# Performance work log

Hardware: AMD Instinct MI355X
Metric: run time of the kernel (lower is better)

The kernel has to match this reference:

```python
import jax, jax.numpy as jnp
import numpy as np
import math

NUM_HEADS = 16
ROPE_BASE = 10000.0


def apply_rope(t):
    # t: [B, H, S, D] with D even. Interleaved-pair rotary embedding (torchtune-style).
    D = t.shape[-1]
    S = t.shape[-2]
    inv_freq = 1.0 / (ROPE_BASE ** (jnp.arange(0, D, 2, dtype=jnp.float32) / D))  # [D/2]
    angles = jnp.arange(S, dtype=jnp.float32)[:, None] * inv_freq[None, :]  # [S, D/2]
    cos = jnp.cos(angles).astype(t.dtype)  # [S, D/2]
    sin = jnp.sin(angles).astype(t.dtype)
    t1 = t[..., 0::2]  # [B, H, S, D/2]
    t2 = t[..., 1::2]
    r1 = t1 * cos - t2 * sin
    r2 = t1 * sin + t2 * cos
    # interleave back
    out = jnp.stack([r1, r2], axis=-1).reshape(t.shape)
    return out


def setup_inputs() -> dict:
    key = jax.random.key(0)
    ks = jax.random.split(key, 6)
    B, S, D = 4, 2048, 2048
    s_in = 1.0 / math.sqrt(D)
    x = jax.random.normal(ks[0], (B, S, D), dtype=jnp.float32)
    wq = jax.random.normal(ks[1], (D, D), dtype=jnp.float32) * s_in
    wk = jax.random.normal(ks[2], (D, D), dtype=jnp.float32) * s_in
    wv = jax.random.normal(ks[3], (D, D), dtype=jnp.float32) * s_in
    wo = jax.random.normal(ks[4], (D, D), dtype=jnp.float32) * s_in
    bo = jnp.zeros((D,), dtype=jnp.float32)
    return {"x": x, "wq": wq, "wk": wk, "wv": wv, "wo": wo, "bo": bo}


def reference(x, wq, wk, wv, wo, bo):
    B, S, D = x.shape
    H = NUM_HEADS
    hd = D // H
    # QKV projections (nn.Linear: y = x @ W^T)
    q = (x @ wq.T).reshape(B, S, H, hd).transpose(0, 2, 1, 3)  # [B,H,S,hd]
    k = (x @ wk.T).reshape(B, S, H, hd).transpose(0, 2, 1, 3)
    v = (x @ wv.T).reshape(B, S, H, hd).transpose(0, 2, 1, 3)
    q = apply_rope(q)
    k = apply_rope(k)
    # causal SDPA (dropout_p = 0 in eval)
    scale = 1.0 / math.sqrt(hd)
    scores = jnp.einsum('bhqd,bhkd->bhqk', q, k) * scale  # [B,H,S,S]
    causal = jnp.tril(jnp.ones((S, S), dtype=bool))
    scores = jnp.where(causal, scores, jnp.finfo(scores.dtype).min)
    attn = jax.nn.softmax(scores, axis=-1)
    ctx = jnp.einsum('bhqk,bhkd->bqhd', attn, v).reshape(B, S, D)
    return ctx @ wo.T + bo
```

## Files before the change

kernel.cpp:

```cpp
#include <hip/hip_runtime.h>

typedef short short8 __attribute__((ext_vector_type(8)));
typedef float f32x4 __attribute__((ext_vector_type(4)));
typedef unsigned int u32x4 __attribute__((ext_vector_type(4)));
typedef unsigned short u16x4 __attribute__((ext_vector_type(4)));
typedef unsigned short u16x8 __attribute__((ext_vector_type(8)));

__device__ __forceinline__ unsigned short f2bf(float f) {
  unsigned int u = __builtin_bit_cast(unsigned int, f);
  u += 0x7fffu + ((u >> 16) & 1u);
  return (unsigned short)(u >> 16);
}
__device__ __forceinline__ float bf2f(unsigned short h) {
  unsigned int u = ((unsigned int)h) << 16;
  return __builtin_bit_cast(float, u);
}

__device__ __forceinline__ void gl16(const unsigned short* g, unsigned short* l) {
  __builtin_amdgcn_global_load_lds((const __attribute__((address_space(1))) unsigned int*)g,
                                   (__attribute__((address_space(3))) unsigned int*)l, 16, 0, 0);
}

#define BB 4
#define SS 2048
#define DD 2048
#define HH 16
#define HD 128
#define MM (BB * SS)

__global__ void cast_all(const float* __restrict__ x, const float* __restrict__ wq,
                         const float* __restrict__ wk, const float* __restrict__ wv,
                         const float* __restrict__ wo, unsigned short* __restrict__ xb,
                         unsigned short* __restrict__ wqb, unsigned short* __restrict__ wkb,
                         unsigned short* __restrict__ wvb, unsigned short* __restrict__ wob) {
  int i = blockIdx.x * blockDim.x + threadIdx.x;
  const int X4 = (MM * DD) / 4;
  const int W4 = (DD * DD) / 4;
  const float* src;
  unsigned short* dst;
  int off;
  if (i < X4) {
    src = x; dst = xb; off = i;
  } else {
    int t = i - X4;
    int w = t >> 20;
    off = t & (W4 - 1);
    src = (w == 0) ? wq : (w == 1) ? wk : (w == 2) ? wv : wo;
    dst = (w == 0) ? wqb : (w == 1) ? wkb : (w == 2) ? wvb : wob;
  }
  f32x4 v = ((const f32x4*)src)[off];
  u16x4 o;
  o[0] = f2bf(v[0]); o[1] = f2bf(v[1]); o[2] = f2bf(v[2]); o[3] = f2bf(v[3]);
  ((u16x4*)dst)[off] = o;
}

#define STGH(P, R0, t, h, moff)                                                     \
  do {                                                                              \
    const unsigned short* _s =                                                      \
        (P) + (size_t)((R0) + (h) * 128 + srow) * DD + (size_t)((t) * 64 + scol);   \
    gl16(_s, lds + (moff) + (h) * 8192 + wvi * 512);                                \
    gl16(_s + (size_t)64 * DD, lds + (moff) + (h) * 8192 + 4096 + wvi * 512);       \
  } while (0)

#define BARRIER asm volatile("s_barrier" ::: "memory")

__device__ __forceinline__ void gemm_core(const unsigned short* __restrict__ Ap,
                                          const unsigned short* __restrict__ Bp,
                                          unsigned short* lds, int rt, int ct,
                                          f32x4 (&acc)[8][4]) {
  const int tid = threadIdx.x;
  const int lane = tid & 63, wvi = tid >> 6;
  const int wm = wvi >> 2, wn = wvi & 3;
  const int quad = lane >> 4, l16 = lane & 15;
  const int srow = wvi * 8 + (lane >> 3);
  const int scol = ((lane & 7) ^ (lane >> 3)) << 3;
  const int ck0 = (quad ^ (l16 & 7)) << 3;
  const int ck1 = ((4 + quad) ^ (l16 & 7)) << 3;
  const int aro = (wm * 128 + l16) << 6;
  const int bro = (wn * 64 + l16) << 6;
  const int rb = rt * 256, cb = ct * 256;

#pragma unroll
  for (int i = 0; i < 8; ++i)
#pragma unroll
    for (int j = 0; j < 4; ++j) acc[i][j] = f32x4{0.f, 0.f, 0.f, 0.f};

  STGH(Bp, cb, 0, 0, 16384);
  STGH(Bp, cb, 0, 1, 16384);
  STGH(Ap, rb, 0, 0, 0);
  STGH(Ap, rb, 0, 1, 0);
  STGH(Bp, cb, 1, 0, 49152);
  STGH(Bp, cb, 1, 1, 49152);
  asm volatile("s_waitcnt vmcnt(4)" ::: "memory");
  BARRIER;

#pragma unroll 2
  for (int t = 0; t < 32; ++t) {
    const unsigned short* ab = lds + ((t & 1) << 15);
    const unsigned short* bb = ab + 16384;
    const int pn = ((t + 1) & 1) << 15;
    const int pc = ((t & 1) << 15) + 16384;
    short8 aq[4][2], b0f[2][2], b1f[2][2];

#pragma unroll
    for (int mi = 0; mi < 4; ++mi) {
      aq[mi][0] = __builtin_bit_cast(short8, *(const u32x4*)(ab + aro + mi * 1024 + ck0));
      aq[mi][1] = __builtin_bit_cast(short8, *(const u32x4*)(ab + aro + mi * 1024 + ck1));
    }
#pragma unroll
    for (int ni = 0; ni < 2; ++ni) {
      b0f[ni][0] = __builtin_bit_cast(short8, *(const u32x4*)(bb + bro + ni * 1024 + ck0));
      b0f[ni][1] = __builtin_bit_cast(short8, *(const u32x4*)(bb + bro + ni * 1024 + ck1));
    }
    if (t < 31) STGH(Ap, rb, t + 1, 0, pn);
    BARRIER;
    __builtin_amdgcn_s_setprio(1);
#pragma unroll
    for (int k = 0; k < 2; ++k)
#pragma unroll
      for (int mi = 0; mi < 4; ++mi)
#pragma unroll
        for (int ni = 0; ni < 2; ++ni)
          acc[mi][ni] =
              __builtin_amdgcn_mfma_f32_16x16x32_bf16(aq[mi][k], b0f[ni][k], acc[mi][ni], 0, 0, 0);
    __builtin_amdgcn_s_setprio(0);
    BARRIER;

#pragma unroll
    for (int ni = 0; ni < 2; ++ni) {
      b1f[ni][0] = __builtin_bit_cast(short8, *(const u32x4*)(bb + bro + 2048 + ni * 1024 + ck0));
      b1f[ni][1] = __builtin_bit_cast(short8, *(const u32x4*)(bb + bro + 2048 + ni * 1024 + ck1));
    }
    if (t < 31) STGH(Ap, rb, t + 1, 1, pn);
    BARRIER;
    __builtin_amdgcn_s_setprio(1);
#pragma unroll
    for (int k = 0; k < 2; ++k)
#pragma unroll
      for (int mi = 0; mi < 4; ++mi)
#pragma unroll
        for (int ni = 0; ni < 2; ++ni)
          acc[mi][2 + ni] = __builtin_amdgcn_mfma_f32_16x16x32_bf16(aq[mi][k], b1f[ni][k],
                                                                    acc[mi][2 + ni], 0, 0, 0);
    __builtin_amdgcn_s_setprio(0);
    BARRIER;

#pragma unroll
    for (int mi = 0; mi < 4; ++mi) {
      aq[mi][0] = __builtin_bit_cast(short8, *(const u32x4*)(ab + aro + 4096 + mi * 1024 + ck0));
      aq[mi][1] = __builtin_bit_cast(short8, *(const u32x4*)(ab + aro + 4096 + mi * 1024 + ck1));
    }
    if (t < 30) STGH(Bp, cb, t + 2, 0, pc);
    BARRIER;
    __builtin_amdgcn_s_setprio(1);
#pragma unroll
    for (int k = 0; k < 2; ++k)
#pragma unroll
      for (int mi = 0; mi < 4; ++mi)
#pragma unroll
        for (int ni = 0; ni < 2; ++ni)
          acc[4 + mi][2 + ni] = __builtin_amdgcn_mfma_f32_16x16x32_bf16(
              aq[mi][k], b1f[ni][k], acc[4 + mi][2 + ni], 0, 0, 0);
    __builtin_amdgcn_s_setprio(0);
    BARRIER;

    if (t < 30) STGH(Bp, cb, t + 2, 1, pc);
    BARRIER;
    __builtin_amdgcn_s_setprio(1);
#pragma unroll
    for (int k = 0; k < 2; ++k)
#pragma unroll
      for (int mi = 0; mi < 4; ++mi)
#pragma unroll
        for (int ni = 0; ni < 2; ++ni)
          acc[4 + mi][ni] = __builtin_amdgcn_mfma_f32_16x16x32_bf16(aq[mi][k], b0f[ni][k],
                                                                    acc[4 + mi][ni], 0, 0, 0);
    __builtin_amdgcn_s_setprio(0);
    if (t < 30) {
      asm volatile("s_waitcnt vmcnt(4)" ::: "memory");
      BARRIER;
    } else if (t == 30) {
      asm volatile("s_waitcnt vmcnt(0)" ::: "memory");
      BARRIER;
    }
  }
}

__global__ __launch_bounds__(512, 2) void gemm_qkv(const unsigned short* __restrict__ A,
                                                   const unsigned short* __restrict__ W0,
                                                   const unsigned short* __restrict__ W1,
                                                   const unsigned short* __restrict__ W2,
                                                   unsigned short* __restrict__ q_out,
                                                   unsigned short* __restrict__ k_out,
                                                   unsigned short* __restrict__ v_out) {
  __shared__ unsigned short lds[65536];
  const int ct = blockIdx.x, rt = blockIdx.y, z = blockIdx.z;
  const unsigned short* W = (z == 0) ? W0 : (z == 1) ? W1 : W2;
  unsigned short* outb = (z == 0) ? q_out : (z == 1) ? k_out : v_out;
  f32x4 acc[8][4];
  gemm_core(A, W, lds, rt, ct, acc);

  const int tid = threadIdx.x;
  const int lane = tid & 63, wvi = tid >> 6;
  const int wm = wvi >> 2, wn = wvi & 3;
  const int quad = lane >> 4, l16 = lane & 15;
#pragma unroll
  for (int mi = 0; mi < 8; ++mi)
#pragma unroll
    for (int ni = 0; ni < 4; ++ni)
#pragma unroll
      for (int r = 0; r < 4; ++r) {
        int row_g = rt * 256 + wm * 128 + mi * 16 + quad * 4 + r;
        int col_g = ct * 256 + wn * 64 + ni * 16 + l16;
        float v = acc[mi][ni][r];
        int b = row_g >> 11, s = row_g & (SS - 1);
        int h = col_g >> 7, d = col_g & (HD - 1);
        size_t rowbase = (((size_t)(b * HH + h)) * SS + (size_t)s) * HD;
        if (z == 1) {
          outb[rowbase + (size_t)((((d >> 3) ^ (s & 7)) << 3) | (d & 7))] = f2bf(v);
        } else {
          outb[rowbase + (size_t)d] = f2bf(v);
        }
      }
}

__global__ __launch_bounds__(512, 2) void gemm_out(const unsigned short* __restrict__ A,
                                                   const unsigned short* __restrict__ W,
                                                   float* __restrict__ outf,
                                                   const float* __restrict__ bias) {
  __shared__ unsigned short lds[65536];
  const int ct = blockIdx.x, rt = blockIdx.y;
  f32x4 acc[8][4];
  gemm_core(A, W, lds, rt, ct, acc);

  const int tid = threadIdx.x;
  const int lane = tid & 63, wvi = tid >> 6;
  const int wm = wvi >> 2, wn = wvi & 3;
  const int quad = lane >> 4, l16 = lane & 15;
#pragma unroll
  for (int mi = 0; mi < 8; ++mi)
#pragma unroll
    for (int ni = 0; ni < 4; ++ni)
#pragma unroll
      for (int r = 0; r < 4; ++r) {
        int row_g = rt * 256 + wm * 128 + mi * 16 + quad * 4 + r;
        int col_g = ct * 256 + wn * 64 + ni * 16 + l16;
        outf[(size_t)row_g * DD + col_g] = acc[mi][ni][r] + bias[col_g];
      }
}

__global__ void rope_kernel(unsigned short* __restrict__ qb, unsigned short* __restrict__ kb) {
  int id = blockIdx.x * blockDim.x + threadIdx.x;
  int c = id & 15;
  int s = (id >> 4) & (SS - 1);
  int bhb = id >> 15;
  unsigned short* p;
  float psc;
  if (bhb < 64) {
    p = qb + ((size_t)bhb * SS + s) * HD + c * 8;
    psc = 0.08838834764831845f;
  } else {
    p = kb + ((size_t)(bhb & 63) * SS + s) * HD + ((c ^ (s & 7)) << 3);
    psc = 1.0f;
  }
  u32x4 w = *(u32x4*)p;
  const float nl = -9.210340371976184f / 64.0f;
  u32x4 o;
#pragma unroll
  for (int j = 0; j < 4; ++j) {
    int pi = c * 4 + j;
    float inv = __expf((float)pi * nl);
    float ang = (float)s * inv;
    float cs = __cosf(ang), sn = __sinf(ang);
    float e = bf2f((unsigned short)(w[j] & 0xffffu));
    float od = bf2f((unsigned short)(w[j] >> 16));
    float r1 = (e * cs - od * sn) * psc;
    float r2 = (e * sn + od * cs) * psc;
    o[j] = (unsigned int)f2bf(r1) | ((unsigned int)f2bf(r2) << 16);
  }
  *(u32x4*)p = o;
}

__global__ __launch_bounds__(256, 4) void attn_kernel(const unsigned short* __restrict__ qb,
                                                      const unsigned short* __restrict__ kb,
                                                      const unsigned short* __restrict__ vb,
                                                      unsigned short* __restrict__ ctxb) {
  __shared__ unsigned short Kt[64 * 128];
  __shared__ unsigned short Vt[128 * 72];
  const int tid = threadIdx.x;
  const int g = blockIdx.x;
  const int bh = g >> 5;
  const int qa = 31 - (g & 31);
  const int lane = tid & 63, wvi = tid >> 6;
  const int quad = lane >> 4, l16 = lane & 15;
  const size_t bhq = (size_t)bh * SS * HD;
  const int qg = qa * 64;
  const int qrow = qg + wvi * 16;
  const int b = bh >> 4, h = bh & (HH - 1);
  unsigned short* Pw = Kt + wvi * 1024;
  f32x4 zero = {0.f, 0.f, 0.f, 0.f};

  short8 qf[4];
#pragma unroll
  for (int ks = 0; ks < 4; ++ks)
    qf[ks] = __builtin_bit_cast(
        short8, *(const u32x4*)(qb + bhq + (size_t)(qrow + l16) * HD + ks * 32 + quad * 8));

  f32x4 acc[8];
#pragma unroll
  for (int dt = 0; dt < 8; ++dt) acc[dt] = zero;
  float lpart[4] = {0.f, 0.f, 0.f, 0.f};

  const int ntile = qa + 1;
  for (int kt = 0; kt < ntile; ++kt) {
    const int kv0 = kt * 64;
    __syncthreads();
#pragma unroll
    for (int r = 0; r < 4; ++r)
      gl16(kb + bhq + (size_t)(kv0 + r * 16 + wvi * 4 + (lane >> 4)) * HD + (lane & 15) * 8,
           Kt + (r * 16 + wvi * 4) * 128);
    for (int u = tid; u < 512; u += 256) {
      int rr = u & 31, c = u >> 5;
      const unsigned short* vsrc = vb + bhq + (size_t)(kv0 + 2 * rr) * HD + c * 8;
      u16x8 va = __builtin_bit_cast(u16x8, *(const u32x4*)vsrc);
      u16x8 vb2 = __builtin_bit_cast(u16x8, *(const u32x4*)(vsrc + HD));
      unsigned int* vw = (unsigned int*)Vt;
#pragma unroll
      for (int j = 0; j < 8; ++j)
        vw[(c * 8 + j) * 36 + rr] = (unsigned int)va[j] | ((unsigned int)vb2[j] << 16);
    }
    __syncthreads();

    f32x4 sc[4];
#pragma unroll
    for (int nt = 0; nt < 4; ++nt) {
      sc[nt] = zero;
#pragma unroll
      for (int ks = 0; ks < 4; ++ks) {
        short8 kf = __builtin_bit_cast(
            short8, *(const u32x4*)(Kt + (nt * 16 + l16) * 128 +
                                    (((ks * 4 + quad) ^ (l16 & 7)) << 3)));
        sc[nt] = __builtin_amdgcn_mfma_f32_16x16x32_bf16(qf[ks], kf, sc[nt], 0, 0, 0);
      }
    }
    __syncthreads();

    const bool dm = (kt == ntile - 1);
    if (dm) {
#pragma unroll
      for (int r = 0; r < 4; ++r) {
        int row = qrow + quad * 4 + r;
        int prow = quad * 4 + r;
#pragma unroll
        for (int nt = 0; nt < 4; ++nt) {
          int col = nt * 16 + l16;
          float pv = (kv0 + col > row) ? 0.f : __expf(sc[nt][r]);
          lpart[r] += pv;
          int el = prow * 64 +
                   ((((nt * 2 + (l16 >> 3)) + prow + 4 * (prow >> 3)) & 7) << 3) + (l16 & 7);
          Pw[el] = f2bf(pv);
        }
      }
    } else {
#pragma unroll
      for (int r = 0; r < 4; ++r) {
        int prow = quad * 4 + r;
#pragma unroll
        for (int nt = 0; nt < 4; ++nt) {
          float pv = __expf(sc[nt][r]);
          lpart[r] += pv;
          int el = prow * 64 +
                   ((((nt * 2 + (l16 >> 3)) + prow + 4 * (prow >> 3)) & 7) << 3) + (l16 & 7);
          Pw[el] = f2bf(pv);
        }
      }
    }

#pragma unroll
    for (int ks2 = 0; ks2 < 2; ++ks2) {
      short8 pf = __builtin_bit_cast(
          short8, *(const u32x4*)(Pw + l16 * 64 +
                                  ((((ks2 * 4 + quad) + l16 + 4 * (l16 >> 3)) & 7) << 3)));
#pragma unroll
      for (int dt = 0; dt < 8; ++dt) {
        short8 vf = __builtin_bit_cast(
            short8, *(const u32x4*)(Vt + (dt * 16 + l16) * 72 + ks2 * 32 + quad * 8));
        acc[dt] = __builtin_amdgcn_mfma_f32_16x16x32_bf16(pf, vf, acc[dt], 0, 0, 0);
      }
    }
  }

  float rl[4];
#pragma unroll
  for (int r = 0; r < 4; ++r) {
    float rs = lpart[r];
#pragma unroll
    for (int off = 1; off < 16; off <<= 1) rs += __shfl_xor(rs, off, 64);
    rl[r] = 1.0f / rs;
  }
#pragma unroll
  for (int dt = 0; dt < 8; ++dt)
#pragma unroll
    for (int r = 0; r < 4; ++r) {
      int row = qrow + quad * 4 + r;
      ctxb[((size_t)(b * SS + row)) * DD + h * HD + dt * 16 + l16] = f2bf(acc[dt][r] * rl[r]);
    }
}

extern "C" void kernel_launch(void* const* d_in, const int* in_sizes, int n_in,
                              void* d_out, int out_size, void* d_ws, size_t ws_size,
                              hipStream_t stream) {
  const float* x = (const float*)d_in[0];
  const float* wq = (const float*)d_in[1];
  const float* wk = (const float*)d_in[2];
  const float* wv = (const float*)d_in[3];
  const float* wo = (const float*)d_in[4];
  const float* bo = (const float*)d_in[5];
  float* out = (float*)d_out;

  unsigned short* xb = (unsigned short*)d_ws;
  unsigned short* wqb = xb + (size_t)MM * DD;
  unsigned short* wkb = wqb + (size_t)DD * DD;
  unsigned short* wvb = wkb + (size_t)DD * DD;
  unsigned short* wob = wvb + (size_t)DD * DD;
  unsigned short* qb = wob + (size_t)DD * DD;
  unsigned short* kb = qb + (size_t)MM * DD;
  unsigned short* vb = kb + (size_t)MM * DD;
  unsigned short* ctxb = vb + (size_t)MM * DD;

  cast_all<<<(2 * MM * DD / 4) / 256, 256, 0, stream>>>(x, wq, wk, wv, wo, xb, wqb, wkb, wvb, wob);

  dim3 gg(DD / 256, MM / 256, 3);
  gemm_qkv<<<gg, 512, 0, stream>>>(xb, wqb, wkb, wvb, qb, kb, vb);

  rope_kernel<<<(128 * 2048 * 16) / 256, 256, 0, stream>>>(qb, kb);

  attn_kernel<<<2048, 256, 0, stream>>>(qb, kb, vb, ctxb);

  dim3 go(DD / 256, MM / 256);
  gemm_out<<<go, 512, 0, stream>>>(ctxb, wob, out, bo);
}
```

Before: 648.2 us.

## Process 128 query rows per attention block to reuse K/V tiles

Each attention workgroup now handles 128 query rows (32 per wave, as two 16-row MFMA blocks) instead of 64, so every K/V tile loaded into LDS feeds twice as many MFMAs and the grid is halved. P gets its own LDS buffer, which removes one barrier per tile, and the V transpose layout switches from padding to an XOR swizzle. The cost is more registers and LDS per block, with launch bounds lowered to 3 waves per SIMD. Fewer blocks and coarser causal tiles may also leave more load imbalance and wasted masked work on the diagonal.

Measured after the change: 747.6 us. 1.15x slower.

```diff
diff --git a/kernel.cpp b/kernel.cpp
--- a/kernel.cpp
+++ b/kernel.cpp
@@ -281,37 +281,42 @@
   *(u32x4*)p = o;
 }
 
-__global__ __launch_bounds__(256, 4) void attn_kernel(const unsigned short* __restrict__ qb,
+__global__ __launch_bounds__(256, 3) void attn_kernel(const unsigned short* __restrict__ qb,
                                                       const unsigned short* __restrict__ kb,
                                                       const unsigned short* __restrict__ vb,
                                                       unsigned short* __restrict__ ctxb) {
   __shared__ unsigned short Kt[64 * 128];
-  __shared__ unsigned short Vt[128 * 72];
+  __shared__ unsigned short Vt[128 * 64];
+  __shared__ unsigned short Pl[4 * 32 * 64];
   const int tid = threadIdx.x;
   const int g = blockIdx.x;
-  const int bh = g >> 5;
-  const int qa = 31 - (g & 31);
+  const int bh = g >> 4;
+  const int qa = 15 - (g & 15);
   const int lane = tid & 63, wvi = tid >> 6;
   const int quad = lane >> 4, l16 = lane & 15;
   const size_t bhq = (size_t)bh * SS * HD;
-  const int qg = qa * 64;
-  const int qrow = qg + wvi * 16;
+  const int qrow = qa * 128 + wvi * 32;
   const int b = bh >> 4, h = bh & (HH - 1);
-  unsigned short* Pw = Kt + wvi * 1024;
+  unsigned short* Pw = Pl + wvi * 2048;
   f32x4 zero = {0.f, 0.f, 0.f, 0.f};
 
-  short8 qf[4];
-#pragma unroll
-  for (int ks = 0; ks < 4; ++ks)
-    qf[ks] = __builtin_bit_cast(
-        short8, *(const u32x4*)(qb + bhq + (size_t)(qrow + l16) * HD + ks * 32 + quad * 8));
-
-  f32x4 acc[8];
-#pragma unroll
-  for (int dt = 0; dt < 8; ++dt) acc[dt] = zero;
-  float lpart[4] = {0.f, 0.f, 0.f, 0.f};
-
-  const int ntile = qa + 1;
+  short8 qf[2][4];
+#pragma unroll
+  for (int rb = 0; rb < 2; ++rb)
+#pragma unroll
+    for (int ks = 0; ks < 4; ++ks)
+      qf[rb][ks] = __builtin_bit_cast(
+          short8,
+          *(const u32x4*)(qb + bhq + (size_t)(qrow + rb * 16 + l16) * HD + ks * 32 + quad * 8));
+
+  f32x4 acc[2][8];
+#pragma unroll
+  for (int rb = 0; rb < 2; ++rb)
+#pragma unroll
+    for (int dt = 0; dt < 8; ++dt) acc[rb][dt] = zero;
+  float lpart[2][4] = {{0.f, 0.f, 0.f, 0.f}, {0.f, 0.f, 0.f, 0.f}};
+
+  const int ntile = 2 * qa + 2;
   for (int kt = 0; kt < ntile; ++kt) {
     const int kv0 = kt * 64;
     __syncthreads();
@@ -327,84 +332,87 @@
       unsigned int* vw = (unsigned int*)Vt;
 #pragma unroll
       for (int j = 0; j < 8; ++j)
-        vw[(c * 8 + j) * 36 + rr] = (unsigned int)va[j] | ((unsigned int)vb2[j] << 16);
+        vw[(c * 8 + j) * 32 + (((rr >> 2) ^ j) << 2) + (rr & 3)] =
+            (unsigned int)va[j] | ((unsigned int)vb2[j] << 16);
     }
     __syncthreads();
 
-    f32x4 sc[4];
+    const bool dm = (kt >= ntile - 2);
 #pragma unroll
     for (int nt = 0; nt < 4; ++nt) {
-      sc[nt] = zero;
+      f32x4 sc0 = zero, sc1 = zero;
 #pragma unroll
       for (int ks = 0; ks < 4; ++ks) {
         short8 kf = __builtin_bit_cast(
             short8, *(const u32x4*)(Kt + (nt * 16 + l16) * 128 +
                                     (((ks * 4 + quad) ^ (l16 & 7)) << 3)));
-        sc[nt] = __builtin_amdgcn_mfma_f32_16x16x32_bf16(qf[ks], kf, sc[nt], 0, 0, 0);
-      }
-    }
-    __syncthreads();
-
-    const bool dm = (kt == ntile - 1);
-    if (dm) {
-#pragma unroll
-      for (int r = 0; r < 4; ++r) {
-        int row = qrow + quad * 4 + r;
-        int prow = quad * 4 + r;
-#pragma unroll
-        for (int nt = 0; nt < 4; ++nt) {
-          int col = nt * 16 + l16;
-          float pv = (kv0 + col > row) ? 0.f : __expf(sc[nt][r]);
-          lpart[r] += pv;
-          int el = prow * 64 +
-                   ((((nt * 2 + (l16 >> 3)) + prow + 4 * (prow >> 3)) & 7) << 3) + (l16 & 7);
-          Pw[el] = f2bf(pv);
+        sc0 = __builtin_amdgcn_mfma_f32_16x16x32_bf16(qf[0][ks], kf, sc0, 0, 0, 0);
+        sc1 = __builtin_amdgcn_mfma_f32_16x16x32_bf16(qf[1][ks], kf, sc1, 0, 0, 0);
+      }
+      const int cc = nt * 2 + (l16 >> 3);
+      if (dm) {
+#pragma unroll
+        for (int r = 0; r < 4; ++r) {
+          int p15 = quad * 4 + r;
+          int col = kv0 + nt * 16 + l16;
+          int el = p15 * 64 + (((cc + p15 + 4 * (p15 >> 3)) & 7) << 3) + (l16 & 7);
+          float pv0 = (col > qrow + p15) ? 0.f : __expf(sc0[r]);
+          lpart[0][r] += pv0;
+          Pw[el] = f2bf(pv0);
+          float pv1 = (col > qrow + 16 + p15) ? 0.f : __expf(sc1[r]);
+          lpart[1][r] += pv1;
+          Pw[1024 + el] = f2bf(pv1);
         }
-      }
-    } else {
-#pragma unroll
-      for (int r = 0; r < 4; ++r) {
-        int prow = quad * 4 + r;
-#pragma unroll
-        for (int nt = 0; nt < 4; ++nt) {
-          float pv = __expf(sc[nt][r]);
-          lpart[r] += pv;
-          int el = prow * 64 +
-                   ((((nt * 2 + (l16 >> 3)) + prow + 4 * (prow >> 3)) & 7) << 3) + (l16 & 7);
-          Pw[el] = f2bf(pv);
+      } else {
+#pragma unroll
+        for (int r = 0; r < 4; ++r) {
+          int p15 = quad * 4 + r;
+          int el = p15 * 64 + (((cc + p15 + 4 * (p15 >> 3)) & 7) << 3) + (l16 & 7);
+          float pv0 = __expf(sc0[r]);
+          lpart[0][r] += pv0;
+          Pw[el] = f2bf(pv0);
+          float pv1 = __expf(sc1[r]);
+          lpart[1][r] += pv1;
+          Pw[1024 + el] = f2bf(pv1);
         }
       }
     }
 
 #pragma unroll
     for (int ks2 = 0; ks2 < 2; ++ks2) {
-      short8 pf = __builtin_bit_cast(
-          short8, *(const u32x4*)(Pw + l16 * 64 +
-                                  ((((ks2 * 4 + quad) + l16 + 4 * (l16 >> 3)) & 7) << 3)));
+      const int pk = (((ks2 * 4 + quad) + l16 + 4 * (l16 >> 3)) & 7) << 3;
+      short8 pf0 = __builtin_bit_cast(short8, *(const u32x4*)(Pw + l16 * 64 + pk));
+      short8 pf1 = __builtin_bit_cast(short8, *(const u32x4*)(Pw + 1024 + l16 * 64 + pk));
 #pragma unroll
       for (int dt = 0; dt < 8; ++dt) {
         short8 vf = __builtin_bit_cast(
-            short8, *(const u32x4*)(Vt + (dt * 16 + l16) * 72 + ks2 * 32 + quad * 8));
-        acc[dt] = __builtin_amdgcn_mfma_f32_16x16x32_bf16(pf, vf, acc[dt], 0, 0, 0);
-      }
-    }
-  }
-
-  float rl[4];
-#pragma unroll
-  for (int r = 0; r < 4; ++r) {
-    float rs = lpart[r];
-#pragma unroll
-    for (int off = 1; off < 16; off <<= 1) rs += __shfl_xor(rs, off, 64);
-    rl[r] = 1.0f / rs;
-  }
-#pragma unroll
-  for (int dt = 0; dt < 8; ++dt)
+            short8, *(const u32x4*)(Vt + (dt * 16 + l16) * 64 +
+                                    (((ks2 * 4 + quad) ^ (l16 & 7)) << 3)));
+        acc[0][dt] = __builtin_amdgcn_mfma_f32_16x16x32_bf16(pf0, vf, acc[0][dt], 0, 0, 0);
+        acc[1][dt] = __builtin_amdgcn_mfma_f32_16x16x32_bf16(pf1, vf, acc[1][dt], 0, 0, 0);
+      }
+    }
+  }
+
+#pragma unroll
+  for (int rb = 0; rb < 2; ++rb) {
+    float rl[4];
 #pragma unroll
     for (int r = 0; r < 4; ++r) {
-      int row = qrow + quad * 4 + r;
-      ctxb[((size_t)(b * SS + row)) * DD + h * HD + dt * 16 + l16] = f2bf(acc[dt][r] * rl[r]);
-    }
+      float rs = lpart[rb][r];
+#pragma unroll
+      for (int off = 1; off < 16; off <<= 1) rs += __shfl_xor(rs, off, 64);
+      rl[r] = 1.0f / rs;
+    }
+#pragma unroll
+    for (int dt = 0; dt < 8; ++dt)
+#pragma unroll
+      for (int r = 0; r < 4; ++r) {
+        int row = qrow + rb * 16 + quad * 4 + r;
+        ctxb[((size_t)(b * SS + row)) * DD + h * HD + dt * 16 + l16] =
+            f2bf(acc[rb][dt][r] * rl[r]);
+      }
+  }
 }
 
 extern "C" void kernel_launch(void* const* d_in, const int* in_sizes, int n_in,
@@ -435,7 +443,7 @@
 
   rope_kernel<<<(128 * 2048 * 16) / 256, 256, 0, stream>>>(qb, kb);
 
-  attn_kernel<<<2048, 256, 0, stream>>>(qb, kb, vb, ctxb);
+  attn_kernel<<<1024, 256, 0, stream>>>(qb, kb, vb, ctxb);
 
   dim3 go(DD / 256, MM / 256);
   gemm_out<<<go, 512, 0, stream>>>(ctxb, wob, out, bo);
```

## Pre-transpose V in QKV epilogue and read K/V directly from global in attention

Applied to the files above, without the earlier changes.

The QKV GEMM epilogue now writes V transposed ([bh, d, s]) through an LDS staging pass, and stops swizzling the K layout. The attention kernel drops its shared-memory K/V tiles and the block-wide barriers, loading MFMA fragments for K and the transposed V straight from global memory (relying on L2/L1 reuse across the four waves). It also remaps block indices so that blocks from different heads interleave. This removes the LDS staging and sync overhead and the in-kernel V transpose, at the cost of redundant global and cache traffic per wave and an extra LDS round trip in the V epilogue.

Measured after the change: 1.064 ms. +64.1%, slower.

```diff
diff --git a/kernel.cpp b/kernel.cpp
--- a/kernel.cpp
+++ b/kernel.cpp
@@ -204,24 +204,58 @@
   const int lane = tid & 63, wvi = tid >> 6;
   const int wm = wvi >> 2, wn = wvi & 3;
   const int quad = lane >> 4, l16 = lane & 15;
-#pragma unroll
-  for (int mi = 0; mi < 8; ++mi)
-#pragma unroll
-    for (int ni = 0; ni < 4; ++ni)
-#pragma unroll
-      for (int r = 0; r < 4; ++r) {
-        int row_g = rt * 256 + wm * 128 + mi * 16 + quad * 4 + r;
-        int col_g = ct * 256 + wn * 64 + ni * 16 + l16;
-        float v = acc[mi][ni][r];
-        int b = row_g >> 11, s = row_g & (SS - 1);
-        int h = col_g >> 7, d = col_g & (HD - 1);
-        size_t rowbase = (((size_t)(b * HH + h)) * SS + (size_t)s) * HD;
-        if (z == 1) {
-          outb[rowbase + (size_t)((((d >> 3) ^ (s & 7)) << 3) | (d & 7))] = f2bf(v);
-        } else {
-          outb[rowbase + (size_t)d] = f2bf(v);
+
+  if (z != 2) {
+#pragma unroll
+    for (int mi = 0; mi < 8; ++mi)
+#pragma unroll
+      for (int ni = 0; ni < 4; ++ni)
+#pragma unroll
+        for (int r = 0; r < 4; ++r) {
+          int row_g = rt * 256 + wm * 128 + mi * 16 + quad * 4 + r;
+          int col_g = ct * 256 + wn * 64 + ni * 16 + l16;
+          int b = row_g >> 11, s = row_g & (SS - 1);
+          int h = col_g >> 7, d = col_g & (HD - 1);
+          outb[(((size_t)(b * HH + h)) * SS + (size_t)s) * HD + (size_t)d] = f2bf(acc[mi][ni][r]);
         }
-      }
+  } else {
+    const int b = rt >> 3;
+    const int s_base = (rt & 7) * 256;
+    const int hbase = ct * 2;
+#pragma unroll
+    for (int nh = 0; nh < 2; ++nh) {
+      __syncthreads();
+      if (((wvi >> 1) & 1) == nh) {
+        const int halfc = (wvi & 1) * 64;
+#pragma unroll
+        for (int mi = 0; mi < 8; ++mi)
+#pragma unroll
+          for (int ni = 0; ni < 4; ++ni)
+#pragma unroll
+            for (int r = 0; r < 4; ++r) {
+              int row_l = wm * 128 + mi * 16 + quad * 4 + r;
+              int cl = halfc + ni * 16 + l16;
+              lds[row_l * 128 + ((((cl >> 3) ^ (row_l & 15)) << 3) | (cl & 7))] =
+                  f2bf(acc[mi][ni][r]);
+            }
+      }
+      __syncthreads();
+      const int d_l = tid >> 2;
+      const int sb = tid & 3;
+      unsigned short* vt =
+          v_out + ((size_t)(b * HH + hbase + nh) * HD + (size_t)d_l) * SS + s_base + sb * 64;
+#pragma unroll
+      for (int j = 0; j < 8; ++j) {
+        u16x8 o8;
+#pragma unroll
+        for (int e = 0; e < 8; ++e) {
+          int row_l = sb * 64 + j * 8 + e;
+          o8[e] = lds[row_l * 128 + ((((d_l >> 3) ^ (row_l & 15)) << 3) | (d_l & 7))];
+        }
+        *(u32x4*)(vt + j * 8) = __builtin_bit_cast(u32x4, o8);
+      }
+    }
+  }
 }
 
 __global__ __launch_bounds__(512, 2) void gemm_out(const unsigned short* __restrict__ A,
@@ -254,15 +288,9 @@
   int c = id & 15;
   int s = (id >> 4) & (SS - 1);
   int bhb = id >> 15;
-  unsigned short* p;
-  float psc;
-  if (bhb < 64) {
-    p = qb + ((size_t)bhb * SS + s) * HD + c * 8;
-    psc = 0.08838834764831845f;
-  } else {
-    p = kb + ((size_t)(bhb & 63) * SS + s) * HD + ((c ^ (s & 7)) << 3);
-    psc = 1.0f;
-  }
+  unsigned short* base = (bhb < 64) ? qb : kb;
+  float psc = (bhb < 64) ? 0.08838834764831845f : 1.0f;
+  unsigned short* p = base + ((size_t)(bhb & 63) * SS + s) * HD + c * 8;
   u32x4 w = *(u32x4*)p;
   const float nl = -9.210340371976184f / 64.0f;
   u32x4 o;
@@ -285,19 +313,18 @@
                                                       const unsigned short* __restrict__ kb,
                                                       const unsigned short* __restrict__ vb,
                                                       unsigned short* __restrict__ ctxb) {
-  __shared__ unsigned short Kt[64 * 128];
-  __shared__ unsigned short Vt[128 * 72];
+  __shared__ unsigned short Pl[4 * 1024];
   const int tid = threadIdx.x;
-  const int g = blockIdx.x;
+  const int g0 = blockIdx.x;
+  const int g = (g0 & 7) * 256 + (g0 >> 3);
   const int bh = g >> 5;
   const int qa = 31 - (g & 31);
   const int lane = tid & 63, wvi = tid >> 6;
   const int quad = lane >> 4, l16 = lane & 15;
   const size_t bhq = (size_t)bh * SS * HD;
-  const int qg = qa * 64;
-  const int qrow = qg + wvi * 16;
+  const int qrow = qa * 64 + wvi * 16;
   const int b = bh >> 4, h = bh & (HH - 1);
-  unsigned short* Pw = Kt + wvi * 1024;
+  unsigned short* Pw = Pl + wvi * 1024;
   f32x4 zero = {0.f, 0.f, 0.f, 0.f};
 
   short8 qf[4];
@@ -314,22 +341,7 @@
   const int ntile = qa + 1;
   for (int kt = 0; kt < ntile; ++kt) {
     const int kv0 = kt * 64;
-    __syncthreads();
-#pragma unroll
-    for (int r = 0; r < 4; ++r)
-      gl16(kb + bhq + (size_t)(kv0 + r * 16 + wvi * 4 + (lane >> 4)) * HD + (lane & 15) * 8,
-           Kt + (r * 16 + wvi * 4) * 128);
-    for (int u = tid; u < 512; u += 256) {
-      int rr = u & 31, c = u >> 5;
-      const unsigned short* vsrc = vb + bhq + (size_t)(kv0 + 2 * rr) * HD + c * 8;
-      u16x8 va = __builtin_bit_cast(u16x8, *(const u32x4*)vsrc);
-      u16x8 vb2 = __builtin_bit_cast(u16x8, *(const u32x4*)(vsrc + HD));
-      unsigned int* vw = (unsigned int*)Vt;
-#pragma unroll
-      for (int j = 0; j < 8; ++j)
-        vw[(c * 8 + j) * 36 + rr] = (unsigned int)va[j] | ((unsigned int)vb2[j] << 16);
-    }
-    __syncthreads();
+    const bool dm = (kt == ntile - 1);
 
     f32x4 sc[4];
 #pragma unroll
@@ -338,14 +350,12 @@
 #pragma unroll
       for (int ks = 0; ks < 4; ++ks) {
         short8 kf = __builtin_bit_cast(
-            short8, *(const u32x4*)(Kt + (nt * 16 + l16) * 128 +
-                                    (((ks * 4 + quad) ^ (l16 & 7)) << 3)));
+            short8, *(const u32x4*)(kb + bhq + (size_t)(kv0 + nt * 16 + l16) * HD + ks * 32 +
+                                    quad * 8));
         sc[nt] = __builtin_amdgcn_mfma_f32_16x16x32_bf16(qf[ks], kf, sc[nt], 0, 0, 0);
       }
     }
-    __syncthreads();
-
-    const bool dm = (kt == ntile - 1);
+
     if (dm) {
 #pragma unroll
       for (int r = 0; r < 4; ++r) {
@@ -384,7 +394,8 @@
 #pragma unroll
       for (int dt = 0; dt < 8; ++dt) {
         short8 vf = __builtin_bit_cast(
-            short8, *(const u32x4*)(Vt + (dt * 16 + l16) * 72 + ks2 * 32 + quad * 8));
+            short8, *(const u32x4*)(vb + bhq + (size_t)(dt * 16 + l16) * SS + kv0 + ks2 * 32 +
+                                    quad * 8));
         acc[dt] = __builtin_amdgcn_mfma_f32_16x16x32_bf16(pf, vf, acc[dt], 0, 0, 0);
       }
     }
```

## Double-buffer K/V tiles in attention and use 128-row query blocks

Applied to the files above, without the earlier changes.

The attention kernel now handles 128 query rows per 512-thread block instead of 64, which halves how often each K/V tile is reloaded. K/V tiles are double-buffered in LDS, so the next tile's global loads are issued before compute on the current one, and the loop needs one barrier per iteration instead of three. V is stored with an XOR swizzle instead of padding, and the block index is remapped across groups of eight, apparently to spread blocks across XCDs. The costs are more LDS per block, lower occupancy (2 blocks/CU), and prefetched V held in registers.

After: 572.6 us. 1.13x faster.

```diff
diff --git a/kernel.cpp b/kernel.cpp
--- a/kernel.cpp
+++ b/kernel.cpp
@@ -281,23 +281,25 @@
   *(u32x4*)p = o;
 }
 
-__global__ __launch_bounds__(256, 4) void attn_kernel(const unsigned short* __restrict__ qb,
+__global__ __launch_bounds__(512, 2) void attn_kernel(const unsigned short* __restrict__ qb,
                                                       const unsigned short* __restrict__ kb,
                                                       const unsigned short* __restrict__ vb,
                                                       unsigned short* __restrict__ ctxb) {
-  __shared__ unsigned short Kt[64 * 128];
-  __shared__ unsigned short Vt[128 * 72];
+  __shared__ unsigned short lds[40960];
   const int tid = threadIdx.x;
-  const int g = blockIdx.x;
-  const int bh = g >> 5;
-  const int qa = 31 - (g & 31);
+  const int g0 = blockIdx.x;
+  const int g = (g0 & 7) * 128 + (g0 >> 3);
+  const int bh = g >> 4;
+  const int qa = 15 - (g & 15);
   const int lane = tid & 63, wvi = tid >> 6;
   const int quad = lane >> 4, l16 = lane & 15;
   const size_t bhq = (size_t)bh * SS * HD;
-  const int qg = qa * 64;
-  const int qrow = qg + wvi * 16;
+  const int qrow = qa * 128 + wvi * 16;
   const int b = bh >> 4, h = bh & (HH - 1);
-  unsigned short* Pw = Kt + wvi * 1024;
+  unsigned short* Pw = lds + 32768 + wvi * 1024;
+  const int vrr = tid & 31, vcd = tid >> 5;
+  const int krow = wvi * 4 + (lane >> 4);
+  const int kcol = (lane & 15) * 8;
   f32x4 zero = {0.f, 0.f, 0.f, 0.f};
 
   short8 qf[4];
@@ -311,25 +313,41 @@
   for (int dt = 0; dt < 8; ++dt) acc[dt] = zero;
   float lpart[4] = {0.f, 0.f, 0.f, 0.f};
 
-  const int ntile = qa + 1;
+  const int ntile = 2 * qa + 2;
+
+  {
+    const unsigned short* vsrc = vb + bhq + (size_t)(2 * vrr) * HD + vcd * 8;
+    u32x4 pva = *(const u32x4*)vsrc;
+    u32x4 pvb = *(const u32x4*)(vsrc + HD);
+    gl16(kb + bhq + (size_t)krow * HD + kcol, lds + krow * 128);
+    gl16(kb + bhq + (size_t)(32 + krow) * HD + kcol, lds + (32 + krow) * 128);
+    u16x8 va = __builtin_bit_cast(u16x8, pva);
+    u16x8 vb2 = __builtin_bit_cast(u16x8, pvb);
+    unsigned int* vw = (unsigned int*)(lds + 16384);
+#pragma unroll
+    for (int j = 0; j < 8; ++j)
+      vw[(vcd * 8 + j) * 32 + (((vrr >> 2) ^ j) << 2) + (vrr & 3)] =
+          (unsigned int)va[j] | ((unsigned int)vb2[j] << 16);
+    __syncthreads();
+  }
+
   for (int kt = 0; kt < ntile; ++kt) {
     const int kv0 = kt * 64;
-    __syncthreads();
-#pragma unroll
-    for (int r = 0; r < 4; ++r)
-      gl16(kb + bhq + (size_t)(kv0 + r * 16 + wvi * 4 + (lane >> 4)) * HD + (lane & 15) * 8,
-           Kt + (r * 16 + wvi * 4) * 128);
-    for (int u = tid; u < 512; u += 256) {
-      int rr = u & 31, c = u >> 5;
-      const unsigned short* vsrc = vb + bhq + (size_t)(kv0 + 2 * rr) * HD + c * 8;
-      u16x8 va = __builtin_bit_cast(u16x8, *(const u32x4*)vsrc);
-      u16x8 vb2 = __builtin_bit_cast(u16x8, *(const u32x4*)(vsrc + HD));
-      unsigned int* vw = (unsigned int*)Vt;
-#pragma unroll
-      for (int j = 0; j < 8; ++j)
-        vw[(c * 8 + j) * 36 + rr] = (unsigned int)va[j] | ((unsigned int)vb2[j] << 16);
-    }
-    __syncthreads();
+    const int cur = (kt & 1) * 8192;
+    const int nxt = ((kt + 1) & 1) * 8192;
+    const unsigned short* Kc = lds + cur;
+    const unsigned short* Vc = lds + 16384 + cur;
+    const bool hasnext = (kt + 1 < ntile);
+
+    u32x4 pva, pvb;
+    if (hasnext) {
+      const int kvn = kv0 + 64;
+      const unsigned short* vsrc = vb + bhq + (size_t)(kvn + 2 * vrr) * HD + vcd * 8;
+      pva = *(const u32x4*)vsrc;
+      pvb = *(const u32x4*)(vsrc + HD);
+      gl16(kb + bhq + (size_t)(kvn + krow) * HD + kcol, lds + nxt + krow * 128);
+      gl16(kb + bhq + (size_t)(kvn + 32 + krow) * HD + kcol, lds + nxt + (32 + krow) * 128);
+    }
 
     f32x4 sc[4];
 #pragma unroll
@@ -338,14 +356,13 @@
 #pragma unroll
       for (int ks = 0; ks < 4; ++ks) {
         short8 kf = __builtin_bit_cast(
-            short8, *(const u32x4*)(Kt + (nt * 16 + l16) * 128 +
+            short8, *(const u32x4*)(Kc + (nt * 16 + l16) * 128 +
                                     (((ks * 4 + quad) ^ (l16 & 7)) << 3)));
         sc[nt] = __builtin_amdgcn_mfma_f32_16x16x32_bf16(qf[ks], kf, sc[nt], 0, 0, 0);
       }
     }
-    __syncthreads();
-
-    const bool dm = (kt == ntile - 1);
+
+    const bool dm = (kt >= ntile - 2);
     if (dm) {
 #pragma unroll
       for (int r = 0; r < 4; ++r) {
@@ -353,8 +370,8 @@
         int prow = quad * 4 + r;
 #pragma unroll
         for (int nt = 0; nt < 4; ++nt) {
-          int col = nt * 16 + l16;
-          float pv = (kv0 + col > row) ? 0.f : __expf(sc[nt][r]);
+          int col = kv0 + nt * 16 + l16;
+          float pv = (col > row) ? 0.f : __expf(sc[nt][r]);
           lpart[r] += pv;
           int el = prow * 64 +
                    ((((nt * 2 + (l16 >> 3)) + prow + 4 * (prow >> 3)) & 7) << 3) + (l16 & 7);
@@ -378,16 +395,28 @@
 
 #pragma unroll
     for (int ks2 = 0; ks2 < 2; ++ks2) {
-      short8 pf = __builtin_bit_cast(
+      short8 pfrag = __builtin_bit_cast(
           short8, *(const u32x4*)(Pw + l16 * 64 +
                                   ((((ks2 * 4 + quad) + l16 + 4 * (l16 >> 3)) & 7) << 3)));
 #pragma unroll
       for (int dt = 0; dt < 8; ++dt) {
         short8 vf = __builtin_bit_cast(
-            short8, *(const u32x4*)(Vt + (dt * 16 + l16) * 72 + ks2 * 32 + quad * 8));
-        acc[dt] = __builtin_amdgcn_mfma_f32_16x16x32_bf16(pf, vf, acc[dt], 0, 0, 0);
-      }
-    }
+            short8, *(const u32x4*)(Vc + (dt * 16 + l16) * 64 +
+                                    (((ks2 * 4 + quad) ^ (l16 & 7)) << 3)));
+        acc[dt] = __builtin_amdgcn_mfma_f32_16x16x32_bf16(pfrag, vf, acc[dt], 0, 0, 0);
+      }
+    }
+
+    if (hasnext) {
+      u16x8 va = __builtin_bit_cast(u16x8, pva);
+      u16x8 vb2 = __builtin_bit_cast(u16x8, pvb);
+      unsigned int* vw = (unsigned int*)(lds + 16384 + nxt);
+#pragma unroll
+      for (int j = 0; j < 8; ++j)
+        vw[(vcd * 8 + j) * 32 + (((vrr >> 2) ^ j) << 2) + (vrr & 3)] =
+            (unsigned int)va[j] | ((unsigned int)vb2[j] << 16);
+    }
+    __syncthreads();
   }
 
   float rl[4];
@@ -435,7 +464,7 @@
 
   rope_kernel<<<(128 * 2048 * 16) / 256, 256, 0, stream>>>(qb, kb);
 
-  attn_kernel<<<2048, 256, 0, stream>>>(qb, kb, vb, ctxb);
+  attn_kernel<<<1024, 512, 0, stream>>>(qb, kb, vb, ctxb);
 
   dim3 go(DD / 256, MM / 256);
   gemm_out<<<go, 512, 0, stream>>>(ctxb, wob, out, bo);
```
